# Performance work log

Hardware: AMD Instinct MI355X
Metric: run time of the kernel (lower is better)

The kernel has to match this reference:

```python
import jax, jax.numpy as jnp
import numpy as np

B, S, D, H = 64, 128, 1024, 8
DK = D // H  # 128 == S, required by the module's (attn@V)@V quirk
DFF = 2048
EPS = 1e-12


def layernorm(x, w, b):
    u = x.mean(-1, keepdims=True)
    s = ((x - u) ** 2).mean(-1, keepdims=True)
    return w * (x - u) / jnp.sqrt(s + EPS) + b


def setup_inputs() -> dict:
    key = jax.random.key(0)
    ks = jax.random.split(key, 10)
    w = lambda k, shape: jax.random.normal(k, shape, jnp.float32) * 0.02
    return {
        "x": jax.random.normal(ks[0], (B, S, D), jnp.float32),
        "mask": jnp.ones((1, 1, S, S), jnp.int32),
        "Wq": w(ks[1], (D, D)), "bq": jnp.zeros((D,), jnp.float32),
        "Wk": w(ks[2], (D, D)), "bk": jnp.zeros((D,), jnp.float32),
        "Wv": w(ks[3], (D, D)), "bv": jnp.zeros((D,), jnp.float32),
        "Wo": w(ks[4], (D, D)), "bo": jnp.zeros((D,), jnp.float32),
        "ln1_w": jnp.ones((D,), jnp.float32), "ln1_b": jnp.zeros((D,), jnp.float32),
        "W1": w(ks[5], (DFF, D)), "b1": jnp.zeros((DFF,), jnp.float32),
        "W2": w(ks[6], (4 * D, DFF)), "b2": jnp.zeros((4 * D,), jnp.float32),
        "W3": w(ks[7], (D, 4 * D)), "b3": jnp.zeros((D,), jnp.float32),
        "ln2_w": jnp.ones((D,), jnp.float32), "ln2_b": jnp.zeros((D,), jnp.float32),
    }


def reference(x, mask, Wq, bq, Wk, bk, Wv, bv, Wo, bo, ln1_w, ln1_b,
              W1, b1, W2, b2, W3, b3, ln2_w, ln2_b):
    # QKV projections -> [B, H, S, DK]
    Q = (x @ Wq.T + bq).reshape(B, S, H, DK).transpose(0, 2, 1, 3)
    K = (x @ Wk.T + bk).reshape(B, S, H, DK).transpose(0, 2, 1, 3)
    V = (x @ Wv.T + bv).reshape(B, S, H, DK).transpose(0, 2, 1, 3)

    scores = jnp.einsum('bhqd,bhkd->bhqk', Q, K) / jnp.sqrt(jnp.float32(DK))
    scores = jnp.where(mask == 0, jnp.float32(-1e9), scores)
    attn = jax.nn.softmax(scores, axis=-1)  # dropout = identity (eval)
    av = jnp.matmul(attn, V)                 # [B,H,S,DK]
    # Faithful quirk in the source: multiply by V a second time (DK == S).
    ctx = jnp.matmul(av, V)                  # [B,H,S,DK]
    ctx = ctx.transpose(0, 2, 1, 3).reshape(B, S, D)
    attn_out = ctx @ Wo.T + bo

    h = layernorm(x + attn_out, ln1_w, ln1_b)

    f = jax.nn.relu(h @ W1.T + b1)           # [B,S,DFF]
    f = jax.nn.relu(f @ W2.T + b2)           # [B,S,4D]
    f = f @ W3.T + b3                        # [B,S,D]

    return layernorm(h + f, ln2_w, ln2_b)
```

## Files before the change

kernel.cpp:

```cpp
#include <hip/hip_runtime.h>
#include <hip/hip_bf16.h>

using bf16 = __hip_bfloat16;
typedef __attribute__((ext_vector_type(4))) float f32x4;
typedef __attribute__((ext_vector_type(8))) short bf16x8;

__device__ __forceinline__ unsigned short bfbits(float f) {
    bf16 h = __float2bfloat16(f);
    return __builtin_bit_cast(unsigned short, h);
}

__device__ __forceinline__ void g2l16(const void* g, void* l) {
    __builtin_amdgcn_global_load_lds(
        (const __attribute__((address_space(1))) unsigned int*)g,
        (__attribute__((address_space(3))) unsigned int*)l, 16, 0, 0);
}

__global__ void castk(const float* __restrict__ in, bf16* __restrict__ out, int n4) {
    int stride = gridDim.x * blockDim.x;
    for (int i = blockIdx.x * blockDim.x + threadIdx.x; i < n4; i += stride) {
        float4 v = reinterpret_cast<const float4*>(in)[i];
        ushort4 o;
        o.x = bfbits(v.x); o.y = bfbits(v.y); o.z = bfbits(v.z); o.w = bfbits(v.w);
        reinterpret_cast<ushort4*>(out)[i] = o;
    }
}

template<int EPI>
__global__ __launch_bounds__(512, 2)
void gemm256(const bf16* __restrict__ A, const bf16* __restrict__ Bm,
             int N, int K,
             const float* __restrict__ bias0, const float* __restrict__ bias1,
             const float* __restrict__ bias2,
             void* __restrict__ outp,
             bf16* __restrict__ q_o, bf16* __restrict__ k_o, bf16* __restrict__ v_o) {
    __shared__ __align__(16) char lds[98304];
    const int tid = threadIdx.x;
    const int lane = tid & 63, wave = tid >> 6;
    const int rlo = lane & 15, g = lane >> 4;
    const int wr = wave >> 2, wc = wave & 3;
    const int nbn = N >> 8;
    const int nwg = gridDim.x;
    int wg = (int)blockIdx.x;
    wg = (wg & 7) * (nwg >> 3) + (wg >> 3);
    const int bm = wg / nbn, bn = wg % nbn;
    const size_t ldb = (size_t)K * 2;
    const char* abase = (const char*)A + ((size_t)bm << 8) * ldb;
    const char* bbase = (const char*)Bm + ((size_t)bn << 8) * ldb;

    const int P = tid * 16;
    const int R = P >> 7;
    const int qs = (P & 127) ^ ((R & 7) << 4);
    const size_t goff0 = (size_t)(R * 2 + (qs >> 6)) * ldb + (qs & 63);
    const size_t ghalf = (size_t)128 * ldb;

    const int o_in = (((rlo & 1) << 6) | (g << 4)) ^ (((rlo >> 1) & 7) << 4);
    const int aoff = wr * 8192 + (rlo >> 1) * 128 + o_in;
    const int boff = 16384 + (wc >> 1) * 8192 + (wc & 1) * 4096 + (rlo >> 1) * 128 + o_in;

    const f32x4 fz = {0.f, 0.f, 0.f, 0.f};
    f32x4 acc[8][4];
#pragma unroll
    for (int i = 0; i < 8; ++i)
#pragma unroll
        for (int j = 0; j < 4; ++j) acc[i][j] = fz;

    auto stA = [&](int buf, int h, int kt) {
        g2l16(abase + goff0 + (size_t)h * ghalf + (size_t)kt * 64,
              lds + buf * 32768 + h * 8192 + P);
    };
    auto stB = [&](int buf, int h, int kt) {
        g2l16(bbase + goff0 + (size_t)h * ghalf + (size_t)kt * 64,
              lds + buf * 32768 + 16384 + h * 8192 + P);
    };

    stA(0, 0, 0); stA(0, 1, 0); stB(0, 0, 0); stB(0, 1, 0);
    stA(1, 0, 1); stA(1, 1, 1); stB(1, 0, 1); stB(1, 1, 1);
    asm volatile("s_waitcnt vmcnt(4)" ::: "memory");
    __builtin_amdgcn_s_barrier();

    const int NT = K >> 5;
    for (int kt = 0; kt < NT; ++kt) {
        const int buf = kt % 3;
        const int nbuf = (kt + 2) % 3;
        const char* lb = lds + buf * 32768;
        const bool pre = (kt + 2) < NT;

        bf16x8 bfr[4], afr[4];
#pragma unroll
        for (int nf = 0; nf < 4; ++nf)
            bfr[nf] = *reinterpret_cast<const bf16x8*>(lb + nf * 1024 + boff);
#pragma unroll
        for (int i = 0; i < 4; ++i)
            afr[i] = *reinterpret_cast<const bf16x8*>(lb + i * 1024 + aoff);
        if (pre) { stA(nbuf, 0, kt + 2); stA(nbuf, 1, kt + 2); }
        __builtin_amdgcn_s_barrier();
        asm volatile("s_waitcnt lgkmcnt(0)");
        __builtin_amdgcn_s_setprio(1);
#pragma unroll
        for (int i = 0; i < 4; ++i)
#pragma unroll
            for (int nf = 0; nf < 4; ++nf)
                acc[i][nf] = __builtin_amdgcn_mfma_f32_16x16x32_bf16(afr[i], bfr[nf], acc[i][nf], 0, 0, 0);
        __builtin_amdgcn_s_setprio(0);
        __builtin_amdgcn_s_barrier();

#pragma unroll
        for (int i = 0; i < 4; ++i)
            afr[i] = *reinterpret_cast<const bf16x8*>(lb + (4 + i) * 1024 + aoff);
        if (pre) { stB(nbuf, 0, kt + 2); stB(nbuf, 1, kt + 2); }
        if (pre) {
            asm volatile("s_waitcnt vmcnt(4)" ::: "memory");
        } else if (kt + 1 < NT) {
            asm volatile("s_waitcnt vmcnt(0)" ::: "memory");
        }
        __builtin_amdgcn_s_barrier();
        asm volatile("s_waitcnt lgkmcnt(0)");
        __builtin_amdgcn_s_setprio(1);
#pragma unroll
        for (int i = 0; i < 4; ++i)
#pragma unroll
            for (int nf = 0; nf < 4; ++nf)
                acc[4 + i][nf] = __builtin_amdgcn_mfma_f32_16x16x32_bf16(afr[i], bfr[nf], acc[4 + i][nf], 0, 0, 0);
        __builtin_amdgcn_s_setprio(0);
        __builtin_amdgcn_s_barrier();
    }

    const int gm0 = (bm << 8) + wr * 128;
    const int gn0 = (bn << 8) + wc * 64;
#pragma unroll
    for (int mf = 0; mf < 8; ++mf) {
#pragma unroll
        for (int nf = 0; nf < 4; ++nf) {
            const int gnc = gn0 + nf * 16 + rlo;
#pragma unroll
            for (int r = 0; r < 4; ++r) {
                const int gmr = gm0 + mf * 16 + g * 4 + r;
                float val = acc[mf][nf][r];
                if constexpr (EPI == 0) {
                    int t = gnc >> 10;
                    const float* bp = (t == 0) ? bias0 : ((t == 1) ? bias1 : bias2);
                    val += bp[gnc & 1023];
                    bf16* dst = (t == 0) ? q_o : ((t == 1) ? k_o : v_o);
                    int hh = (gnc >> 7) & 7, d = gnc & 127;
                    int bb = gmr >> 7, s = gmr & 127;
                    dst[(((size_t)bb * 8 + hh) * 128 + s) * 128 + d] = __float2bfloat16(val);
                } else {
                    val = fmaxf(val + bias0[gnc], 0.f);
                    ((bf16*)outp)[(size_t)gmr * N + gnc] = __float2bfloat16(val);
                }
            }
        }
    }
}

template<int EPI>
__global__ __launch_bounds__(256, 2)
void gemm_bt(const bf16* __restrict__ A, const bf16* __restrict__ Bm,
             int M, int N, int K,
             const float* __restrict__ bias0, const float* __restrict__ resid,
             void* __restrict__ outp) {
    (void)M;
    __shared__ __align__(16) char As[8192];
    __shared__ __align__(16) char Bs[8192];
    int tid = threadIdx.x, wave = tid >> 6, lane = tid & 63;
    int nbn = N >> 7;
    int bm = blockIdx.x / nbn, bn = blockIdx.x % nbn;
    int wm = (wave >> 1) << 6, wn = (wave & 1) << 6;
    int rlo = lane & 15, g = lane >> 4;

    const char* abase = (const char*)(A + (size_t)(bm << 7) * K);
    const char* bbase = (const char*)(Bm + (size_t)(bn << 7) * K);

    const f32x4 fzero = {0.f, 0.f, 0.f, 0.f};
    f32x4 acc[4][4];
#pragma unroll
    for (int i = 0; i < 4; ++i)
#pragma unroll
        for (int j = 0; j < 4; ++j) acc[i][j] = fzero;

    int L0 = wave * 2048 + lane * 16;
    size_t ldbyte = (size_t)K * 2;

    for (int k0 = 0; k0 < K; k0 += 32) {
#pragma unroll
        for (int j = 0; j < 2; ++j) {
            int L = L0 + j * 1024;
            int row = L >> 6;
            int cb = (L & 63) ^ (((row >> 1) & 3) << 4);
            g2l16(abase + (size_t)row * ldbyte + (size_t)k0 * 2 + cb, As + wave * 2048 + j * 1024);
            g2l16(bbase + (size_t)row * ldbyte + (size_t)k0 * 2 + cb, Bs + wave * 2048 + j * 1024);
        }
        __syncthreads();
        bf16x8 af[4], bf8[4];
#pragma unroll
        for (int i = 0; i < 4; ++i) {
            int ra = wm + i * 16 + rlo;
            af[i] = *reinterpret_cast<const bf16x8*>(As + ra * 64 + ((g * 16) ^ (((ra >> 1) & 3) << 4)));
            int rb = wn + i * 16 + rlo;
            bf8[i] = *reinterpret_cast<const bf16x8*>(Bs + rb * 64 + ((g * 16) ^ (((rb >> 1) & 3) << 4)));
        }
#pragma unroll
        for (int mi = 0; mi < 4; ++mi)
#pragma unroll
            for (int ni = 0; ni < 4; ++ni)
                acc[mi][ni] = __builtin_amdgcn_mfma_f32_16x16x32_bf16(af[mi], bf8[ni], acc[mi][ni], 0, 0, 0);
        __syncthreads();
    }

    int gm0 = (bm << 7) + wm, gn0 = (bn << 7) + wn;
#pragma unroll
    for (int mi = 0; mi < 4; ++mi) {
#pragma unroll
        for (int ni = 0; ni < 4; ++ni) {
            int gnc = gn0 + ni * 16 + rlo;
#pragma unroll
            for (int r = 0; r < 4; ++r) {
                int gmr = gm0 + mi * 16 + g * 4 + r;
                float val = acc[mi][ni][r];
                val += bias0[gnc] + resid[(size_t)gmr * N + gnc];
                ((float*)outp)[(size_t)gmr * N + gnc] = val;
            }
        }
    }
}

__global__ __launch_bounds__(256)
void transpose_v(const bf16* __restrict__ V, bf16* __restrict__ VT) {
    __shared__ unsigned short t[128 * 132];
    int bh = blockIdx.x, tid = threadIdx.x;
    const unsigned short* src = (const unsigned short*)(V + (size_t)bh * 16384);
#pragma unroll
    for (int i = 0; i < 8; ++i) {
        int idx = tid + i * 256;
        int srow = idx >> 4;
        int c8 = (idx & 15) * 8;
        ushort4 a = reinterpret_cast<const ushort4*>(src + srow * 128 + c8)[0];
        ushort4 b = reinterpret_cast<const ushort4*>(src + srow * 128 + c8 + 4)[0];
        reinterpret_cast<ushort4*>(t + srow * 132 + c8)[0] = a;
        reinterpret_cast<ushort4*>(t + srow * 132 + c8 + 4)[0] = b;
    }
    __syncthreads();
    unsigned short* dst = (unsigned short*)(VT + (size_t)bh * 16384);
#pragma unroll
    for (int i = 0; i < 8; ++i) {
        int idx = tid + i * 256;
        int drow = idx >> 4;
        int s8 = (idx & 15) * 8;
        ushort4 a, b;
        a.x = t[(s8 + 0) * 132 + drow]; a.y = t[(s8 + 1) * 132 + drow];
        a.z = t[(s8 + 2) * 132 + drow]; a.w = t[(s8 + 3) * 132 + drow];
        b.x = t[(s8 + 4) * 132 + drow]; b.y = t[(s8 + 5) * 132 + drow];
        b.z = t[(s8 + 6) * 132 + drow]; b.w = t[(s8 + 7) * 132 + drow];
        reinterpret_cast<ushort4*>(dst + drow * 128 + s8)[0] = a;
        reinterpret_cast<ushort4*>(dst + drow * 128 + s8 + 4)[0] = b;
    }
}

__global__ __launch_bounds__(256, 2)
void attn_scores(const bf16* __restrict__ Q, const bf16* __restrict__ K, bf16* __restrict__ P) {
    __shared__ __align__(16) char Qs[32768];
    __shared__ __align__(16) char Ks[32768];
    int bh = blockIdx.x;
    int tid = threadIdx.x, wave = tid >> 6, lane = tid & 63;
    const char* qsrc = (const char*)(Q + (size_t)bh * 16384);
    const char* ksrc = (const char*)(K + (size_t)bh * 16384);
#pragma unroll
    for (int j = 0; j < 8; ++j) {
        int L = wave * 8192 + j * 1024 + lane * 16;
        int row = L >> 8;
        int cb = (L & 255) ^ ((row & 7) << 4);
        g2l16(qsrc + row * 256 + cb, Qs + wave * 8192 + j * 1024);
        g2l16(ksrc + row * 256 + cb, Ks + wave * 8192 + j * 1024);
    }
    __syncthreads();
    int rlo = lane & 15, g = lane >> 4;
    const f32x4 fzero = {0.f, 0.f, 0.f, 0.f};
    f32x4 acc[2][8];
#pragma unroll
    for (int mi = 0; mi < 2; ++mi)
#pragma unroll
        for (int ni = 0; ni < 8; ++ni) acc[mi][ni] = fzero;
#pragma unroll
    for (int kk = 0; kk < 4; ++kk) {
        bf16x8 aq[2], bk8[8];
#pragma unroll
        for (int mi = 0; mi < 2; ++mi) {
            int row = wave * 32 + mi * 16 + rlo;
            aq[mi] = *reinterpret_cast<const bf16x8*>(Qs + row * 256 + ((kk * 64 + g * 16) ^ ((row & 7) << 4)));
        }
#pragma unroll
        for (int ni = 0; ni < 8; ++ni) {
            int row = ni * 16 + rlo;
            bk8[ni] = *reinterpret_cast<const bf16x8*>(Ks + row * 256 + ((kk * 64 + g * 16) ^ ((row & 7) << 4)));
        }
#pragma unroll
        for (int mi = 0; mi < 2; ++mi)
#pragma unroll
            for (int ni = 0; ni < 8; ++ni)
                acc[mi][ni] = __builtin_amdgcn_mfma_f32_16x16x32_bf16(aq[mi], bk8[ni], acc[mi][ni], 0, 0, 0);
    }
    const float scale = 0.088388347648318447f;
    unsigned short* pdst = (unsigned short*)(P + (size_t)bh * 16384);
#pragma unroll
    for (int mi = 0; mi < 2; ++mi) {
#pragma unroll
        for (int r = 0; r < 4; ++r) {
            float m = -3e38f;
#pragma unroll
            for (int ni = 0; ni < 8; ++ni) m = fmaxf(m, acc[mi][ni][r]);
#pragma unroll
            for (int o = 1; o < 16; o <<= 1) m = fmaxf(m, __shfl_xor(m, o));
            m *= scale;
            float e[8];
            float sum = 0.f;
#pragma unroll
            for (int ni = 0; ni < 8; ++ni) { e[ni] = __expf(acc[mi][ni][r] * scale - m); sum += e[ni]; }
#pragma unroll
            for (int o = 1; o < 16; o <<= 1) sum += __shfl_xor(sum, o);
            float inv = 1.f / sum;
            int qrow = wave * 32 + mi * 16 + g * 4 + r;
#pragma unroll
            for (int ni = 0; ni < 8; ++ni)
                pdst[qrow * 128 + ni * 16 + rlo] = bfbits(e[ni] * inv);
        }
    }
}

__global__ __launch_bounds__(256, 2)
void attn_ctx(const bf16* __restrict__ P, const bf16* __restrict__ VT, bf16* __restrict__ CTX) {
    __shared__ __align__(16) char Vs[32768];
    __shared__ __align__(16) char Ts[32768];
    int bh = blockIdx.x, b = bh >> 3, h = bh & 7;
    int tid = threadIdx.x, wave = tid >> 6, lane = tid & 63;
    const char* vsrc = (const char*)(VT + (size_t)bh * 16384);
#pragma unroll
    for (int j = 0; j < 8; ++j) {
        int L = wave * 8192 + j * 1024 + lane * 16;
        int row = L >> 8;
        int cb = (L & 255) ^ ((row & 7) << 4);
        g2l16(vsrc + row * 256 + cb, Vs + wave * 8192 + j * 1024);
    }
    __syncthreads();
    int rlo = lane & 15, g = lane >> 4;
    const char* psrc = (const char*)(P + (size_t)bh * 16384);
    const f32x4 fzero = {0.f, 0.f, 0.f, 0.f};
    f32x4 accT[2][8];
#pragma unroll
    for (int mi = 0; mi < 2; ++mi)
#pragma unroll
        for (int ni = 0; ni < 8; ++ni) accT[mi][ni] = fzero;
#pragma unroll
    for (int kk = 0; kk < 4; ++kk) {
        bf16x8 ap[2], bv8[8];
#pragma unroll
        for (int mi = 0; mi < 2; ++mi) {
            int row = wave * 32 + mi * 16 + rlo;
            ap[mi] = *reinterpret_cast<const bf16x8*>(psrc + (size_t)row * 256 + kk * 64 + g * 16);
        }
#pragma unroll
        for (int ni = 0; ni < 8; ++ni) {
            int row = ni * 16 + rlo;
            bv8[ni] = *reinterpret_cast<const bf16x8*>(Vs + row * 256 + ((kk * 64 + g * 16) ^ ((row & 7) << 4)));
        }
#pragma unroll
        for (int mi = 0; mi < 2; ++mi)
#pragma unroll
            for (int ni = 0; ni < 8; ++ni)
                accT[mi][ni] = __builtin_amdgcn_mfma_f32_16x16x32_bf16(ap[mi], bv8[ni], accT[mi][ni], 0, 0, 0);
    }
#pragma unroll
    for (int mi = 0; mi < 2; ++mi)
#pragma unroll
        for (int ni = 0; ni < 8; ++ni)
#pragma unroll
            for (int r = 0; r < 4; ++r) {
                int trow = wave * 32 + mi * 16 + g * 4 + r;
                int cbyte = ((ni * 16 + rlo) * 2) ^ ((trow & 7) << 4);
                *(unsigned short*)(Ts + trow * 256 + cbyte) = bfbits(accT[mi][ni][r]);
            }
    __syncthreads();
    f32x4 accC[2][8];
#pragma unroll
    for (int mi = 0; mi < 2; ++mi)
#pragma unroll
        for (int ni = 0; ni < 8; ++ni) accC[mi][ni] = fzero;
#pragma unroll
    for (int kk = 0; kk < 4; ++kk) {
        bf16x8 at[2], bv8[8];
#pragma unroll
        for (int mi = 0; mi < 2; ++mi) {
            int row = wave * 32 + mi * 16 + rlo;
            at[mi] = *reinterpret_cast<const bf16x8*>(Ts + row * 256 + ((kk * 64 + g * 16) ^ ((row & 7) << 4)));
        }
#pragma unroll
        for (int ni = 0; ni < 8; ++ni) {
            int row = ni * 16 + rlo;
            bv8[ni] = *reinterpret_cast<const bf16x8*>(Vs + row * 256 + ((kk * 64 + g * 16) ^ ((row & 7) << 4)));
        }
#pragma unroll
        for (int mi = 0; mi < 2; ++mi)
#pragma unroll
            for (int ni = 0; ni < 8; ++ni)
                accC[mi][ni] = __builtin_amdgcn_mfma_f32_16x16x32_bf16(at[mi], bv8[ni], accC[mi][ni], 0, 0, 0);
    }
    unsigned short* cdst = (unsigned short*)CTX;
#pragma unroll
    for (int mi = 0; mi < 2; ++mi)
#pragma unroll
        for (int ni = 0; ni < 8; ++ni)
#pragma unroll
            for (int r = 0; r < 4; ++r) {
                int q = wave * 32 + mi * 16 + g * 4 + r;
                int gm = b * 128 + q;
                int col = h * 128 + ni * 16 + rlo;
                cdst[(size_t)gm * 1024 + col] = bfbits(accC[mi][ni][r]);
            }
}

template<int MODE>
__global__ __launch_bounds__(256)
void ln_k(const float* __restrict__ Y, const float* __restrict__ w, const float* __restrict__ b,
          float* __restrict__ Hf, bf16* __restrict__ Hb) {
    int row = blockIdx.x, tid = threadIdx.x;
    float4 v = reinterpret_cast<const float4*>(Y + (size_t)row * 1024)[tid];
    float s = v.x + v.y + v.z + v.w;
    float q = v.x * v.x + v.y * v.y + v.z * v.z + v.w * v.w;
#pragma unroll
    for (int o = 1; o < 64; o <<= 1) { s += __shfl_xor(s, o); q += __shfl_xor(q, o); }
    __shared__ float ss[4], sq[4];
    if ((tid & 63) == 0) { ss[tid >> 6] = s; sq[tid >> 6] = q; }
    __syncthreads();
    s = ss[0] + ss[1] + ss[2] + ss[3];
    q = sq[0] + sq[1] + sq[2] + sq[3];
    float u = s * (1.f / 1024.f);
    float var = fmaxf(q * (1.f / 1024.f) - u * u, 0.f);
    float rstd = rsqrtf(var + 1e-12f);
    float4 wv = reinterpret_cast<const float4*>(w)[tid];
    float4 bv = reinterpret_cast<const float4*>(b)[tid];
    float o0 = wv.x * (v.x - u) * rstd + bv.x;
    float o1 = wv.y * (v.y - u) * rstd + bv.y;
    float o2 = wv.z * (v.z - u) * rstd + bv.z;
    float o3 = wv.w * (v.w - u) * rstd + bv.w;
    reinterpret_cast<float4*>(Hf + (size_t)row * 1024)[tid] = make_float4(o0, o1, o2, o3);
    if constexpr (MODE == 0) {
        ushort4 ob;
        ob.x = bfbits(o0); ob.y = bfbits(o1); ob.z = bfbits(o2); ob.w = bfbits(o3);
        reinterpret_cast<ushort4*>(Hb)[row * 256 + tid] = ob;
    }
}

extern "C" void kernel_launch(void* const* d_in, const int* in_sizes, int n_in,
                              void* d_out, int out_size, void* d_ws, size_t ws_size,
                              hipStream_t stream) {
    (void)in_sizes; (void)n_in; (void)out_size; (void)ws_size;
    const float* x    = (const float*)d_in[0];
    const float* Wq   = (const float*)d_in[2];
    const float* bq   = (const float*)d_in[3];
    const float* Wk   = (const float*)d_in[4];
    const float* bk   = (const float*)d_in[5];
    const float* Wv   = (const float*)d_in[6];
    const float* bv   = (const float*)d_in[7];
    const float* Wo   = (const float*)d_in[8];
    const float* bo   = (const float*)d_in[9];
    const float* ln1w = (const float*)d_in[10];
    const float* ln1b = (const float*)d_in[11];
    const float* W1   = (const float*)d_in[12];
    const float* b1   = (const float*)d_in[13];
    const float* W2   = (const float*)d_in[14];
    const float* b2   = (const float*)d_in[15];
    const float* W3   = (const float*)d_in[16];
    const float* b3   = (const float*)d_in[17];
    const float* ln2w = (const float*)d_in[18];
    const float* ln2b = (const float*)d_in[19];

    char* ws = (char*)d_ws;
    bf16*  XB    = (bf16*)(ws + 0);
    bf16*  WQKVB = (bf16*)(ws + 16777216);
    bf16*  WOB   = (bf16*)(ws + 23068672);
    bf16*  W1B   = (bf16*)(ws + 25165824);
    bf16*  W2B   = (bf16*)(ws + 29360128);
    bf16*  W3B   = (bf16*)(ws + 46137344);
    bf16*  Qb    = (bf16*)(ws + 54525952);
    bf16*  Kb    = (bf16*)(ws + 71303168);
    bf16*  Vb    = (bf16*)(ws + 88080384);
    bf16*  VTb   = (bf16*)(ws + 104857600);
    bf16*  Pb    = (bf16*)(ws + 121634816);
    bf16*  CTX   = (bf16*)(ws + 138412032);
    float* Y2    = (float*)(ws + 155189248);
    float* H32   = (float*)(ws + 188743680);
    bf16*  HB    = (bf16*)(ws + 222298112);
    bf16*  F1    = (bf16*)(ws + 155189248);
    bf16*  F2    = (bf16*)(ws + 54525952);
    float* Y5    = (float*)(ws + 121634816);

    auto cast = [&](const float* s, bf16* dd, int n4) {
        int nb = (n4 + 255) / 256; if (nb > 2048) nb = 2048;
        castk<<<nb, 256, 0, stream>>>(s, dd, n4);
    };
    cast(x,  XB,             2097152);
    cast(Wq, WQKVB,           262144);
    cast(Wk, WQKVB + 1048576, 262144);
    cast(Wv, WQKVB + 2097152, 262144);
    cast(Wo, WOB,             262144);
    cast(W1, W1B,             524288);
    cast(W2, W2B,            2097152);
    cast(W3, W3B,            1048576);

    gemm256<0><<<384, 512, 0, stream>>>(XB, WQKVB, 3072, 1024,
                                        bq, bk, bv, nullptr, Qb, Kb, Vb);
    transpose_v<<<512, 256, 0, stream>>>(Vb, VTb);
    attn_scores<<<512, 256, 0, stream>>>(Qb, Kb, Pb);
    attn_ctx<<<512, 256, 0, stream>>>(Pb, VTb, CTX);
    gemm_bt<2><<<512, 256, 0, stream>>>(CTX, WOB, 8192, 1024, 1024, bo, x, (void*)Y2);
    ln_k<0><<<8192, 256, 0, stream>>>(Y2, ln1w, ln1b, H32, HB);
    gemm256<1><<<256, 512, 0, stream>>>(HB, W1B, 2048, 1024,
                                        b1, nullptr, nullptr, (void*)F1, nullptr, nullptr, nullptr);
    gemm256<1><<<512, 512, 0, stream>>>(F1, W2B, 4096, 2048,
                                        b2, nullptr, nullptr, (void*)F2, nullptr, nullptr, nullptr);
    gemm_bt<2><<<512, 256, 0, stream>>>(F2, W3B, 8192, 1024, 4096, b3, H32, (void*)Y5);
    ln_k<1><<<8192, 256, 0, stream>>>(Y5, ln2w, ln2b, (float*)d_out, nullptr);
}
```

Before: 475.3 us.

## Use split-K 256-tile GEMM for W3 and fuse partial sum into LayerNorm

The W3 GEMM (K=4096, N=1024) moves from the small gemm_bt kernel to the 256x256 gemm256 kernel with a two-way split-K, each slice writing fp32 partials. A new ln2k kernel sums both partials, adds bias and residual, and applies the final LayerNorm. The main loop also drops two of the four barriers per k-step, keeping one barrier per iteration plus sched_barrier hints, to cut synchronisation stalls. This costs an extra fp32 partial buffer round-trip and relies on the remaining single barrier being enough to protect the LDS triple buffer.

Result: faster. 437.4 us (-8.0%).

```diff
diff --git a/kernel.cpp b/kernel.cpp
--- a/kernel.cpp
+++ b/kernel.cpp
@@ -26,10 +26,10 @@
     }
 }
 
-template<int EPI>
+template<int EPI, int SPLITK>
 __global__ __launch_bounds__(512, 2)
 void gemm256(const bf16* __restrict__ A, const bf16* __restrict__ Bm,
-             int N, int K,
+             int N, int ldk, int kloop,
              const float* __restrict__ bias0, const float* __restrict__ bias1,
              const float* __restrict__ bias2,
              void* __restrict__ outp,
@@ -43,10 +43,16 @@
     const int nwg = gridDim.x;
     int wg = (int)blockIdx.x;
     wg = (wg & 7) * (nwg >> 3) + (wg >> 3);
+    int slice = 0;
+    if constexpr (SPLITK) {
+        int half = nwg >> 1;
+        slice = (wg >= half) ? 1 : 0;
+        wg -= slice * half;
+    }
     const int bm = wg / nbn, bn = wg % nbn;
-    const size_t ldb = (size_t)K * 2;
-    const char* abase = (const char*)A + ((size_t)bm << 8) * ldb;
-    const char* bbase = (const char*)Bm + ((size_t)bn << 8) * ldb;
+    const size_t ldb = (size_t)ldk * 2;
+    const char* abase = (const char*)A + ((size_t)bm << 8) * ldb + (size_t)slice * kloop * 2;
+    const char* bbase = (const char*)Bm + ((size_t)bn << 8) * ldb + (size_t)slice * kloop * 2;
 
     const int P = tid * 16;
     const int R = P >> 7;
@@ -78,12 +84,12 @@
     stA(1, 0, 1); stA(1, 1, 1); stB(1, 0, 1); stB(1, 1, 1);
     asm volatile("s_waitcnt vmcnt(4)" ::: "memory");
     __builtin_amdgcn_s_barrier();
-
-    const int NT = K >> 5;
+    __builtin_amdgcn_sched_barrier(0);
+
+    const int NT = kloop >> 5;
     for (int kt = 0; kt < NT; ++kt) {
-        const int buf = kt % 3;
+        const char* lb = lds + (kt % 3) * 32768;
         const int nbuf = (kt + 2) % 3;
-        const char* lb = lds + buf * 32768;
         const bool pre = (kt + 2) < NT;
 
         bf16x8 bfr[4], afr[4];
@@ -94,7 +100,6 @@
         for (int i = 0; i < 4; ++i)
             afr[i] = *reinterpret_cast<const bf16x8*>(lb + i * 1024 + aoff);
         if (pre) { stA(nbuf, 0, kt + 2); stA(nbuf, 1, kt + 2); }
-        __builtin_amdgcn_s_barrier();
         asm volatile("s_waitcnt lgkmcnt(0)");
         __builtin_amdgcn_s_setprio(1);
 #pragma unroll
@@ -103,27 +108,29 @@
             for (int nf = 0; nf < 4; ++nf)
                 acc[i][nf] = __builtin_amdgcn_mfma_f32_16x16x32_bf16(afr[i], bfr[nf], acc[i][nf], 0, 0, 0);
         __builtin_amdgcn_s_setprio(0);
-        __builtin_amdgcn_s_barrier();
 
 #pragma unroll
         for (int i = 0; i < 4; ++i)
             afr[i] = *reinterpret_cast<const bf16x8*>(lb + (4 + i) * 1024 + aoff);
         if (pre) { stB(nbuf, 0, kt + 2); stB(nbuf, 1, kt + 2); }
+        asm volatile("s_waitcnt lgkmcnt(0)");
+        __builtin_amdgcn_s_setprio(1);
+#pragma unroll
+        for (int i = 0; i < 4; ++i)
+#pragma unroll
+            for (int nf = 0; nf < 4; ++nf)
+                acc[4 + i][nf] = __builtin_amdgcn_mfma_f32_16x16x32_bf16(afr[i], bfr[nf], acc[4 + i][nf], 0, 0, 0);
+        __builtin_amdgcn_s_setprio(0);
+
         if (pre) {
             asm volatile("s_waitcnt vmcnt(4)" ::: "memory");
         } else if (kt + 1 < NT) {
             asm volatile("s_waitcnt vmcnt(0)" ::: "memory");
         }
-        __builtin_amdgcn_s_barrier();
-        asm volatile("s_waitcnt lgkmcnt(0)");
-        __builtin_amdgcn_s_setprio(1);
-#pragma unroll
-        for (int i = 0; i < 4; ++i)
-#pragma unroll
-            for (int nf = 0; nf < 4; ++nf)
-                acc[4 + i][nf] = __builtin_amdgcn_mfma_f32_16x16x32_bf16(afr[i], bfr[nf], acc[4 + i][nf], 0, 0, 0);
-        __builtin_amdgcn_s_setprio(0);
-        __builtin_amdgcn_s_barrier();
+        if (kt + 1 < NT) {
+            __builtin_amdgcn_s_barrier();
+            __builtin_amdgcn_sched_barrier(0);
+        }
     }
 
     const int gm0 = (bm << 8) + wr * 128;
@@ -145,9 +152,12 @@
                     int hh = (gnc >> 7) & 7, d = gnc & 127;
                     int bb = gmr >> 7, s = gmr & 127;
                     dst[(((size_t)bb * 8 + hh) * 128 + s) * 128 + d] = __float2bfloat16(val);
-                } else {
+                } else if constexpr (EPI == 1) {
                     val = fmaxf(val + bias0[gnc], 0.f);
                     ((bf16*)outp)[(size_t)gmr * N + gnc] = __float2bfloat16(val);
+                } else {
+                    float* pp = (float*)outp + (size_t)slice * 8388608;
+                    pp[(size_t)gmr * N + gnc] = val;
                 }
             }
         }
@@ -448,6 +458,41 @@
         ob.x = bfbits(o0); ob.y = bfbits(o1); ob.z = bfbits(o2); ob.w = bfbits(o3);
         reinterpret_cast<ushort4*>(Hb)[row * 256 + tid] = ob;
     }
+}
+
+__global__ __launch_bounds__(256)
+void ln2k(const float* __restrict__ PA, const float* __restrict__ PB,
+          const float* __restrict__ b3, const float* __restrict__ resid,
+          const float* __restrict__ w, const float* __restrict__ b,
+          float* __restrict__ out) {
+    int row = blockIdx.x, tid = threadIdx.x;
+    size_t off = (size_t)row * 256 + tid;
+    float4 pa = reinterpret_cast<const float4*>(PA)[off];
+    float4 pb = reinterpret_cast<const float4*>(PB)[off];
+    float4 bi = reinterpret_cast<const float4*>(b3)[tid];
+    float4 rs = reinterpret_cast<const float4*>(resid)[off];
+    float4 v = make_float4(pa.x + pb.x + bi.x + rs.x, pa.y + pb.y + bi.y + rs.y,
+                           pa.z + pb.z + bi.z + rs.z, pa.w + pb.w + bi.w + rs.w);
+    float s = v.x + v.y + v.z + v.w;
+    float q = v.x * v.x + v.y * v.y + v.z * v.z + v.w * v.w;
+#pragma unroll
+    for (int o = 1; o < 64; o <<= 1) { s += __shfl_xor(s, o); q += __shfl_xor(q, o); }
+    __shared__ float ss[4], sq[4];
+    if ((tid & 63) == 0) { ss[tid >> 6] = s; sq[tid >> 6] = q; }
+    __syncthreads();
+    s = ss[0] + ss[1] + ss[2] + ss[3];
+    q = sq[0] + sq[1] + sq[2] + sq[3];
+    float u = s * (1.f / 1024.f);
+    float var = fmaxf(q * (1.f / 1024.f) - u * u, 0.f);
+    float rstd = rsqrtf(var + 1e-12f);
+    float4 wv = reinterpret_cast<const float4*>(w)[tid];
+    float4 bv = reinterpret_cast<const float4*>(b)[tid];
+    float4 o4;
+    o4.x = wv.x * (v.x - u) * rstd + bv.x;
+    o4.y = wv.y * (v.y - u) * rstd + bv.y;
+    o4.z = wv.z * (v.z - u) * rstd + bv.z;
+    o4.w = wv.w * (v.w - u) * rstd + bv.w;
+    reinterpret_cast<float4*>(out)[off] = o4;
 }
 
 extern "C" void kernel_launch(void* const* d_in, const int* in_sizes, int n_in,
@@ -492,7 +537,8 @@
     bf16*  HB    = (bf16*)(ws + 222298112);
     bf16*  F1    = (bf16*)(ws + 155189248);
     bf16*  F2    = (bf16*)(ws + 54525952);
-    float* Y5    = (float*)(ws + 121634816);
+    float* PW3   = (float*)(ws + 121634816);
+    float* PW3b  = (float*)(ws + 0);
 
     auto cast = [&](const float* s, bf16* dd, int n4) {
         int nb = (n4 + 255) / 256; if (nb > 2048) nb = 2048;
@@ -507,17 +553,19 @@
     cast(W2, W2B,            2097152);
     cast(W3, W3B,            1048576);
 
-    gemm256<0><<<384, 512, 0, stream>>>(XB, WQKVB, 3072, 1024,
-                                        bq, bk, bv, nullptr, Qb, Kb, Vb);
+    gemm256<0, 0><<<384, 512, 0, stream>>>(XB, WQKVB, 3072, 1024, 1024,
+                                           bq, bk, bv, nullptr, Qb, Kb, Vb);
     transpose_v<<<512, 256, 0, stream>>>(Vb, VTb);
     attn_scores<<<512, 256, 0, stream>>>(Qb, Kb, Pb);
     attn_ctx<<<512, 256, 0, stream>>>(Pb, VTb, CTX);
     gemm_bt<2><<<512, 256, 0, stream>>>(CTX, WOB, 8192, 1024, 1024, bo, x, (void*)Y2);
     ln_k<0><<<8192, 256, 0, stream>>>(Y2, ln1w, ln1b, H32, HB);
-    gemm256<1><<<256, 512, 0, stream>>>(HB, W1B, 2048, 1024,
-                                        b1, nullptr, nullptr, (void*)F1, nullptr, nullptr, nullptr);
-    gemm256<1><<<512, 512, 0, stream>>>(F1, W2B, 4096, 2048,
-                                        b2, nullptr, nullptr, (void*)F2, nullptr, nullptr, nullptr);
-    gemm_bt<2><<<512, 256, 0, stream>>>(F2, W3B, 8192, 1024, 4096, b3, H32, (void*)Y5);
-    ln_k<1><<<8192, 256, 0, stream>>>(Y5, ln2w, ln2b, (float*)d_out, nullptr);
-}
+    gemm256<1, 0><<<256, 512, 0, stream>>>(HB, W1B, 2048, 1024, 1024,
+                                           b1, nullptr, nullptr, (void*)F1, nullptr, nullptr, nullptr);
+    gemm256<1, 0><<<512, 512, 0, stream>>>(F1, W2B, 4096, 2048, 2048,
+                                           b2, nullptr, nullptr, (void*)F2, nullptr, nullptr, nullptr);
+    gemm256<2, 1><<<256, 512, 0, stream>>>(F2, W3B, 1024, 4096, 2048,
+                                           nullptr, nullptr, nullptr, (void*)PW3, nullptr, nullptr, nullptr);
+    (void)PW3b;
+    ln2k<<<8192, 256, 0, stream>>>(PW3, PW3 + 8388608, b3, H32, ln2w, ln2b, (float*)d_out);
+}
```
